# Performance work log

Measured on AMD Instinct MI355X. Metric: run time of the kernel, lower is better.

Reference implementation:

```python
import jax, jax.numpy as jnp
import numpy as np

B, T, V, E, H, L = 16384, 100, 256, 50, 10, 15
KEEP = 0.9  # dropout keep prob (drop_rate=0.1)


def setup_inputs() -> dict:
    key = jax.random.key(0)
    ks = jax.random.split(key, 8)
    x = jax.random.randint(ks[0], (B, T), 0, V)
    emb = jax.random.normal(ks[1], (V, E), dtype=jnp.float32) * 0.05
    Wx = jax.random.normal(ks[2], (E, H), dtype=jnp.float32) * (1.0 / np.sqrt(E))
    Wh = jax.random.normal(ks[3], (H, H), dtype=jnp.float32) * (1.0 / np.sqrt(H))
    b_rnn = jnp.zeros((H,), dtype=jnp.float32)
    Wd = jax.random.normal(ks[4], (H, L), dtype=jnp.float32) * (1.0 / np.sqrt(H))
    bd = jnp.zeros((L,), dtype=jnp.float32)
    # inverted dropout mask, deterministic stand-in for tf.nn.dropout(h, drop_rate)
    drop_mask = (jax.random.bernoulli(ks[5], KEEP, (B, H)).astype(jnp.float32) / KEEP)
    return {"x": x, "emb": emb, "Wx": Wx, "Wh": Wh, "b_rnn": b_rnn,
            "Wd": Wd, "bd": bd, "drop_mask": drop_mask}


def reference(x, emb, Wx, Wh, b_rnn, Wd, bd, drop_mask):
    e = emb[x]                      # [B, T, E] embedding lookup
    xs = jnp.transpose(e, (1, 0, 2))  # [T, B, E] for scan over time

    def step(h, xt):                # SimpleRNN cell: h_t = tanh(x_t Wx + h Wh + b)
        h = jnp.tanh(xt @ Wx + h @ Wh + b_rnn)
        return h, None

    h0 = jnp.zeros((x.shape[0], Wh.shape[0]), dtype=emb.dtype)
    hT, _ = jax.lax.scan(step, h0, xs)
    hT = hT * drop_mask             # inverted dropout
    logits = hT @ Wd + bd           # [B, L]
    return logits
```

## Files before the change

kernel.cpp:

```cpp
#include <hip/hip_runtime.h>
#include <hip/hip_bf16.h>


#define Bn 16384
#define Tn 100
#define Vn 256
#define En 50
#define Hn 10
#define Ln 15
#define PROW 12

typedef float v2f __attribute__((ext_vector_type(2)));

#define QP_X1 0xB1
#define QP_X2 0x4E
#define QP_X3 0x1B
#define DPPF(v, ctrl) \
    __int_as_float(__builtin_amdgcn_mov_dpp(__float_as_int(v), (ctrl), 0xF, 0xF, true))

__device__ __forceinline__ float tanh_fast(float x) {
    float xc = fminf(fmaxf(x, -8.f), 8.f);
    float e  = __builtin_amdgcn_exp2f(xc * 2.8853900817779268f);
    float r  = __builtin_amdgcn_rcpf(e + 1.f);
    return __builtin_fmaf(-2.f, r, 1.f);
}

__global__ void precompute_P(const float* __restrict__ emb,
                             const float* __restrict__ Wx,
                             const float* __restrict__ b_rnn,
                             float* __restrict__ P) {
    int tid = blockIdx.x * blockDim.x + threadIdx.x;
    if (tid >= Vn * PROW) return;
    int v = tid / PROW, j = tid - v * PROW;
    float acc = 0.f;
    if (j < Hn) {
        acc = b_rnn[j];
        #pragma unroll 5
        for (int k = 0; k < En; ++k)
            acc = __builtin_fmaf(emb[v * En + k], Wx[k * Hn + j], acc);
    }
    P[tid] = acc;
}

__global__ __launch_bounds__(256) void rnn_fwd(
    const int* __restrict__ x,
    const float* __restrict__ P,
    const float* __restrict__ Wh,
    const float* __restrict__ Wd,
    const float* __restrict__ bd,
    const float* __restrict__ drop,
    float* __restrict__ out) {
    __shared__ float Pl[Vn * PROW];

    {
        const float4* Pg = (const float4*)P;
        float4* Ps = (float4*)Pl;
        #pragma unroll
        for (int i = 0; i < 3; ++i)
            Ps[i * 256 + threadIdx.x] = Pg[i * 256 + threadIdx.x];
    }

    const int g  = blockIdx.x * 256 + threadIdx.x;
    const int b  = g >> 2;
    const int q  = g & 3;
    const int j0 = 3 * q;

    v2f  whv[4][3];
    float whs[4][3];
    #pragma unroll
    for (int m = 0; m < 4; ++m) {
        int qs = q ^ m;
        #pragma unroll
        for (int rp = 0; rp < 3; ++rp) {
            int js  = 3 * qs + rp;
            int jss = js < Hn ? js : 0;
            float w0 = Wh[jss * Hn + (j0 + 0 < Hn ? j0 + 0 : 0)];
            float w1 = Wh[jss * Hn + (j0 + 1 < Hn ? j0 + 1 : 0)];
            float w2 = Wh[jss * Hn + (j0 + 2 < Hn ? j0 + 2 : 0)];
            bool oks = js < Hn;
            v2f wv;
            wv.x = (oks && j0 + 0 < Hn) ? w0 : 0.f;
            wv.y = (oks && j0 + 1 < Hn) ? w1 : 0.f;
            whv[m][rp] = wv;
            whs[m][rp] = (oks && j0 + 2 < Hn) ? w2 : 0.f;
        }
    }
    __syncthreads();

    const int* xb = x + b * Tn;

    v2f  hv = {0.f, 0.f};
    float hs = 0.f;

    int4 xi = *(const int4*)xb;
    for (int c = 0; c < Tn / 4; ++c) {
        int4 xin = (c + 1 < Tn / 4) ? ((const int4*)xb)[c + 1] : xi;
        int xs[4] = {xi.x, xi.y, xi.z, xi.w};
        #pragma unroll
        for (int u = 0; u < 4; ++u) {
            const float* Pr = &Pl[xs[u] * PROW + j0];
            v2f  pv;
            pv.x = Pr[0];
            pv.y = Pr[1];
            float ps = Pr[2];

            float hsrc[4][3];
            hsrc[0][0] = hv.x;            hsrc[0][1] = hv.y;            hsrc[0][2] = hs;
            hsrc[1][0] = DPPF(hv.x, QP_X1); hsrc[1][1] = DPPF(hv.y, QP_X1); hsrc[1][2] = DPPF(hs, QP_X1);
            hsrc[2][0] = DPPF(hv.x, QP_X2); hsrc[2][1] = DPPF(hv.y, QP_X2); hsrc[2][2] = DPPF(hs, QP_X2);
            hsrc[3][0] = DPPF(hv.x, QP_X3); hsrc[3][1] = DPPF(hv.y, QP_X3); hsrc[3][2] = DPPF(hs, QP_X3);

            #pragma unroll
            for (int m = 0; m < 4; ++m)
                #pragma unroll
                for (int rp = 0; rp < 3; ++rp) {
                    v2f hb = {hsrc[m][rp], hsrc[m][rp]};
                    pv += hb * whv[m][rp];
                    ps = __builtin_fmaf(hsrc[m][rp], whs[m][rp], ps);
                }

            hv.x = tanh_fast(pv.x);
            hv.y = tanh_fast(pv.y);
            hs   = tanh_fast(ps);
        }
        xi = xin;
    }

    float hd[3];
    {
        float hown[3] = {hv.x, hv.y, hs};
        #pragma unroll
        for (int r = 0; r < 3; ++r) {
            int j   = j0 + r;
            int jdi = b * Hn + (j < Hn ? j : Hn - 1);
            float d = drop[jdi];
            hd[r] = (j < Hn) ? hown[r] * d : 0.f;
        }
    }
    float hdsrc[4][3];
    hdsrc[0][0] = hd[0];            hdsrc[0][1] = hd[1];            hdsrc[0][2] = hd[2];
    hdsrc[1][0] = DPPF(hd[0], QP_X1); hdsrc[1][1] = DPPF(hd[1], QP_X1); hdsrc[1][2] = DPPF(hd[2], QP_X1);
    hdsrc[2][0] = DPPF(hd[0], QP_X2); hdsrc[2][1] = DPPF(hd[1], QP_X2); hdsrc[2][2] = DPPF(hd[2], QP_X2);
    hdsrc[3][0] = DPPF(hd[0], QP_X3); hdsrc[3][1] = DPPF(hd[1], QP_X3); hdsrc[3][2] = DPPF(hd[2], QP_X3);

    const int l0   = q * 4;
    const int lcnt = (q == 3) ? 3 : 4;
    #pragma unroll
    for (int li = 0; li < 4; ++li) {
        if (li >= lcnt) break;
        int l = l0 + li;
        float acc = bd[l];
        #pragma unroll
        for (int m = 0; m < 4; ++m)
            #pragma unroll
            for (int rp = 0; rp < 3; ++rp) {
                int js  = 3 * (q ^ m) + rp;
                int jss = js < Hn ? js : 0;
                acc = __builtin_fmaf(hdsrc[m][rp], Wd[jss * Ln + l], acc);
            }
        out[b * Ln + l] = acc;
    }
}

extern "C" void kernel_launch(void* const* d_in, const int* in_sizes, int n_in,
                              void* d_out, int out_size, void* d_ws, size_t ws_size,
                              hipStream_t stream) {
    const int*   x      = (const int*)d_in[0];
    const float* emb    = (const float*)d_in[1];
    const float* Wx     = (const float*)d_in[2];
    const float* Wh     = (const float*)d_in[3];
    const float* b_rnn  = (const float*)d_in[4];
    const float* Wd     = (const float*)d_in[5];
    const float* bd     = (const float*)d_in[6];
    const float* drop   = (const float*)d_in[7];
    float*       out    = (float*)d_out;

    float* P = (float*)d_ws;

    precompute_P<<<(Vn * PROW + 255) / 256, 256, 0, stream>>>(emb, Wx, b_rnn, P);
    rnn_fwd<<<(Bn * 4) / 256, 256, 0, stream>>>(x, P, Wh, Wd, bd, drop, out);
}
```

Measured before the change: 90.97 us.

## Fuse embedding-projection precompute into RNN kernel, recompute table per block

Removes the separate precompute_P launch and instead has every block load emb and Wx into shared memory and compute the 256x12 projection table itself before the recurrence. This drops one kernel launch and the global round-trip of the table. The cost is redundant work in all 256 blocks plus about 66 KB of extra shared memory per block, which may lower occupancy. The tanh clamp also switches to a single fmed3 instruction.

```diff
diff --git a/kernel.cpp b/kernel.cpp
--- a/kernel.cpp
+++ b/kernel.cpp
@@ -19,53 +19,77 @@
     __int_as_float(__builtin_amdgcn_mov_dpp(__float_as_int(v), (ctrl), 0xF, 0xF, true))
 
 __device__ __forceinline__ float tanh_fast(float x) {
-    float xc = fminf(fmaxf(x, -8.f), 8.f);
+    float xc = __builtin_amdgcn_fmed3f(x, -8.f, 8.f);
     float e  = __builtin_amdgcn_exp2f(xc * 2.8853900817779268f);
     float r  = __builtin_amdgcn_rcpf(e + 1.f);
     return __builtin_fmaf(-2.f, r, 1.f);
 }
 
-__global__ void precompute_P(const float* __restrict__ emb,
-                             const float* __restrict__ Wx,
-                             const float* __restrict__ b_rnn,
-                             float* __restrict__ P) {
-    int tid = blockIdx.x * blockDim.x + threadIdx.x;
-    if (tid >= Vn * PROW) return;
-    int v = tid / PROW, j = tid - v * PROW;
-    float acc = 0.f;
-    if (j < Hn) {
-        acc = b_rnn[j];
-        #pragma unroll 5
-        for (int k = 0; k < En; ++k)
-            acc = __builtin_fmaf(emb[v * En + k], Wx[k * Hn + j], acc);
-    }
-    P[tid] = acc;
-}
-
-__global__ __launch_bounds__(256) void rnn_fwd(
+__global__ __launch_bounds__(256) void rnn_fused(
     const int* __restrict__ x,
-    const float* __restrict__ P,
+    const float* __restrict__ emb,
+    const float* __restrict__ Wx,
+    const float* __restrict__ b_rnn,
     const float* __restrict__ Wh,
     const float* __restrict__ Wd,
     const float* __restrict__ bd,
     const float* __restrict__ drop,
     float* __restrict__ out) {
+    __shared__ float embL[Vn * En];
+    __shared__ float WxL[(En + 1) * PROW];
     __shared__ float Pl[Vn * PROW];
 
+    const int tid = threadIdx.x;
+
     {
-        const float4* Pg = (const float4*)P;
-        float4* Ps = (float4*)Pl;
-        #pragma unroll
-        for (int i = 0; i < 3; ++i)
-            Ps[i * 256 + threadIdx.x] = Pg[i * 256 + threadIdx.x];
-    }
-
-    const int g  = blockIdx.x * 256 + threadIdx.x;
+        const float4* Eg = (const float4*)emb;
+        float4* Es = (float4*)embL;
+        #pragma unroll
+        for (int i = 0; i < 13; ++i) {
+            int idx = i * 256 + tid;
+            if (idx < (Vn * En) / 4) Es[idx] = Eg[idx];
+        }
+    }
+    for (int i = tid; i < (En + 1) * PROW; i += 256) {
+        int k = i / PROW, j = i - k * PROW;
+        float v = 0.f;
+        if (j < Hn) v = (k < En) ? Wx[k * Hn + j] : b_rnn[j];
+        WxL[i] = v;
+    }
+    __syncthreads();
+
+    {
+        const int v = tid;
+        v2f acc[PROW / 2];
+        {
+            const v2f* brow = (const v2f*)(WxL + En * PROW);
+            #pragma unroll
+            for (int j2 = 0; j2 < PROW / 2; ++j2) acc[j2] = brow[j2];
+        }
+        const v2f* er = (const v2f*)(embL + v * En);
+        #pragma unroll 5
+        for (int k2 = 0; k2 < En / 2; ++k2) {
+            v2f e2 = er[k2];
+            const v2f* w0 = (const v2f*)(WxL + (2 * k2) * PROW);
+            const v2f* w1 = w0 + PROW / 2;
+            v2f ex = {e2.x, e2.x}, ey = {e2.y, e2.y};
+            #pragma unroll
+            for (int j2 = 0; j2 < PROW / 2; ++j2) {
+                acc[j2] += ex * w0[j2];
+                acc[j2] += ey * w1[j2];
+            }
+        }
+        v2f* Pr = (v2f*)(Pl + v * PROW);
+        #pragma unroll
+        for (int j2 = 0; j2 < PROW / 2; ++j2) Pr[j2] = acc[j2];
+    }
+
+    const int g  = blockIdx.x * 256 + tid;
     const int b  = g >> 2;
     const int q  = g & 3;
     const int j0 = 3 * q;
 
-    v2f  whv[4][3];
+    v2f   whv[4][3];
     float whs[4][3];
     #pragma unroll
     for (int m = 0; m < 4; ++m) {
@@ -89,7 +113,7 @@
 
     const int* xb = x + b * Tn;
 
-    v2f  hv = {0.f, 0.f};
+    v2f   hv = {0.f, 0.f};
     float hs = 0.f;
 
     int4 xi = *(const int4*)xb;
@@ -99,13 +123,13 @@
         #pragma unroll
         for (int u = 0; u < 4; ++u) {
             const float* Pr = &Pl[xs[u] * PROW + j0];
-            v2f  pv;
+            v2f pv;
             pv.x = Pr[0];
             pv.y = Pr[1];
             float ps = Pr[2];
 
             float hsrc[4][3];
-            hsrc[0][0] = hv.x;            hsrc[0][1] = hv.y;            hsrc[0][2] = hs;
+            hsrc[0][0] = hv.x;              hsrc[0][1] = hv.y;              hsrc[0][2] = hs;
             hsrc[1][0] = DPPF(hv.x, QP_X1); hsrc[1][1] = DPPF(hv.y, QP_X1); hsrc[1][2] = DPPF(hs, QP_X1);
             hsrc[2][0] = DPPF(hv.x, QP_X2); hsrc[2][1] = DPPF(hv.y, QP_X2); hsrc[2][2] = DPPF(hs, QP_X2);
             hsrc[3][0] = DPPF(hv.x, QP_X3); hsrc[3][1] = DPPF(hv.y, QP_X3); hsrc[3][2] = DPPF(hs, QP_X3);
@@ -138,7 +162,7 @@
         }
     }
     float hdsrc[4][3];
-    hdsrc[0][0] = hd[0];            hdsrc[0][1] = hd[1];            hdsrc[0][2] = hd[2];
+    hdsrc[0][0] = hd[0];              hdsrc[0][1] = hd[1];              hdsrc[0][2] = hd[2];
     hdsrc[1][0] = DPPF(hd[0], QP_X1); hdsrc[1][1] = DPPF(hd[1], QP_X1); hdsrc[1][2] = DPPF(hd[2], QP_X1);
     hdsrc[2][0] = DPPF(hd[0], QP_X2); hdsrc[2][1] = DPPF(hd[1], QP_X2); hdsrc[2][2] = DPPF(hd[2], QP_X2);
     hdsrc[3][0] = DPPF(hd[0], QP_X3); hdsrc[3][1] = DPPF(hd[1], QP_X3); hdsrc[3][2] = DPPF(hd[2], QP_X3);
@@ -174,9 +198,7 @@
     const float* bd     = (const float*)d_in[6];
     const float* drop   = (const float*)d_in[7];
     float*       out    = (float*)d_out;
-
-    float* P = (float*)d_ws;
-
-    precompute_P<<<(Vn * PROW + 255) / 256, 256, 0, stream>>>(emb, Wx, b_rnn, P);
-    rnn_fwd<<<(Bn * 4) / 256, 256, 0, stream>>>(x, P, Wh, Wd, bd, drop, out);
+    (void)d_ws; (void)ws_size;
+
+    rnn_fused<<<(Bn * 4) / 256, 256, 0, stream>>>(x, emb, Wx, b_rnn, Wh, Wd, bd, drop, out);
 }
```

Result: faster. 88.76 us (-2.4%).
